# Kernel optimization log

Measured on AMD Instinct MI355X. Metric: run time of the kernel, lower is better.

Reference implementation:

```python
import jax, jax.numpy as jnp
import numpy as np

B, C, L, N, S = 32, 256, 512, 1024, 8  # batch, channels, seq_len, n_rois, output bins


def setup_inputs() -> dict:
    key = jax.random.key(0)
    k1, k2, k3 = jax.random.split(key, 3)
    sentences = jax.random.normal(k1, (B, C, L, 1), dtype=jnp.float32)
    rois = jnp.sort(jax.random.randint(k2, (N, 2), 0, L, dtype=jnp.int64), axis=1)
    # guarantee non-empty crop: x2 >= x1 + 1 (clamped into [0, L])
    x1 = jnp.minimum(rois[:, 0], L - 1)
    x2 = jnp.clip(rois[:, 1], x1 + 1, L)
    rois = jnp.stack([x1, x2], axis=1)
    roi_idx = jax.random.randint(k3, (N,), 0, B, dtype=jnp.int64)
    return {"sentences": sentences, "rois": rois, "roi_idx": roi_idx}


def reference(sentences, rois, roi_idx):
    # Gather per-ROI sentences; width dim is always sliced [0:1] -> drop it.
    x = sentences[roi_idx, :, :, 0]              # [N, C, L]
    x1 = rois[:, 0]                               # [N]
    x2 = rois[:, 1]                               # [N]
    lr = x2 - x1                                  # per-ROI crop length, >= 1
    pos = jnp.arange(L)[None, :]                  # [1, L]
    bins = []
    for j in range(S):  # fixed small loop over output bins
        # AdaptiveMaxPool bin j: [floor(j*lr/S), ceil((j+1)*lr/S)) offset by x1
        start = x1 + (j * lr) // S                # [N]
        end = x1 + ((j + 1) * lr + S - 1) // S    # [N]
        mask = (pos >= start[:, None]) & (pos < end[:, None])  # [N, L]
        masked = jnp.where(mask[:, None, :], x, -jnp.inf)       # [N, C, L]
        bins.append(masked.max(axis=-1))                         # [N, C]
    out = jnp.stack(bins, axis=-1)[..., None]     # [N, C, S, 1]
    return out
```

## Files before the change

kernel.cpp:

```cpp
#include <hip/hip_runtime.h>
#include <cfloat>

constexpr int Bc = 32;
constexpr int Cc = 256;
constexpr int Lc = 512;
constexpr int Nc = 1024;
constexpr int Sc = 8;

constexpr int CT     = 16;
constexpr int STRIDE = 516;

typedef float f4 __attribute__((ext_vector_type(4)));
typedef float f2 __attribute__((ext_vector_type(2)));

__global__ __launch_bounds__(256) void roi_pool_fused2(
    const float* __restrict__ sentences,
    const int*   __restrict__ rois,
    const int*   __restrict__ roi_idx,
    float*       __restrict__ out)
{
    __shared__ float rowbuf[CT * STRIDE];
    __shared__ int   list[Nc];
    __shared__ int   wcnt[16];

    const int bid  = blockIdx.x;
    const int b    = bid >> 5;
    const int ct   = (bid >> 1) & 15;
    const int half = bid & 1;
    const int c0   = ct * CT;

    const int tid  = threadIdx.x;
    const int lane = tid & 63;
    const int w    = tid >> 6;

    int myidx[4], mypos[4];
    #pragma unroll
    for (int q = 0; q < 4; ++q) {
        const int i = q * 256 + tid;
        const int v = roi_idx[i];
        const unsigned long long mask = __ballot(v == b);
        mypos[q] = __popcll(mask & ((1ull << lane) - 1ull));
        myidx[q] = (v == b) ? i : -1;
        if (lane == 0) wcnt[q * 4 + w] = __popcll(mask);
    }

    {
        const f4* src = (const f4*)(sentences + ((size_t)b * Cc + c0) * Lc);
        #pragma unroll
        for (int i = 0; i < (CT * Lc / 4) / 256; ++i) {
            const int idx = tid + i * 256;
            const int r   = idx >> 7;
            const int q   = idx & 127;
            f4 v = src[r * (Lc / 4) + q];
            *(f4*)(rowbuf + r * STRIDE + 4 * q) = v;
        }
    }
    __syncthreads();

    int wb0 = 0, wb1 = 0, wb2 = 0, wb3 = 0, run = 0;
    #pragma unroll
    for (int t = 0; t < 16; ++t) {
        if (t == w)      wb0 = run;
        if (t == 4 + w)  wb1 = run;
        if (t == 8 + w)  wb2 = run;
        if (t == 12 + w) wb3 = run;
        run += wcnt[t];
    }
    const int m = run;

    if (myidx[0] >= 0) list[wb0 + mypos[0]] = myidx[0];
    if (myidx[1] >= 0) list[wb1 + mypos[1]] = myidx[1];
    if (myidx[2] >= 0) list[wb2 + mypos[2]] = myidx[2];
    if (myidx[3] >= 0) list[wb3 + mypos[3]] = myidx[3];
    __syncthreads();

    const int rp = tid >> 7;
    const int cl = (tid >> 3) & 15;
    const int j  = tid & 7;
    const float* row = rowbuf + cl * STRIDE;

    for (int i = half + 2 * rp; i < m; i += 4) {
        const int n  = list[i];
        const int x1 = rois[2 * n];
        const int x2 = rois[2 * n + 1];
        const int lr = x2 - x1;
        const int s  = x1 + ((j * lr) >> 3);
        const int e  = x1 + (((j + 1) * lr + Sc - 1) >> 3);

        float m0 = -FLT_MAX, m1 = -FLT_MAX;
        int p = s;
        if (p & 1) { m0 = row[p]; ++p; }
        for (; p + 4 <= e; p += 4) {
            f2 a = *(const f2*)(row + p);
            f2 c = *(const f2*)(row + p + 2);
            m0 = fmaxf(m0, fmaxf(a.x, a.y));
            m1 = fmaxf(m1, fmaxf(c.x, c.y));
        }
        if (p + 2 <= e) {
            f2 a = *(const f2*)(row + p);
            m0 = fmaxf(m0, fmaxf(a.x, a.y));
            p += 2;
        }
        if (p < e) m0 = fmaxf(m0, row[p]);

        out[(size_t)n * (Cc * Sc) + (c0 + cl) * Sc + j] = fmaxf(m0, m1);
    }
}

extern "C" void kernel_launch(void* const* d_in, const int* in_sizes, int n_in,
                              void* d_out, int out_size, void* d_ws, size_t ws_size,
                              hipStream_t stream) {
    const float* sentences = (const float*)d_in[0];
    const int*   rois      = (const int*)d_in[1];
    const int*   roi_idx   = (const int*)d_in[2];
    float*       out       = (float*)d_out;

    roi_pool_fused2<<<Bc * (Cc / CT) * 2, 256, 0, stream>>>(sentences, rois, roi_idx, out);
}
```

Measured before the change: 19.71 us.

## Add 4-wide max pyramid level in shared memory and drop half-split blocks

While staging each channel tile into shared memory, the kernel now also stores a per-4-element max level. Each bin reduction then handles only the partial 4-element chunks at its ends with masked vector reads and takes the interior from the reduced level, which cuts LDS reads and max operations for long bins. The grid is halved: each block now processes all of its batch's ROIs instead of splitting them across two blocks, so the global staging of the tile is no longer duplicated. In exchange, fewer blocks are in flight, each block does more serial ROI iterations, and shared-memory use per block rises slightly.

```diff
diff --git a/kernel.cpp b/kernel.cpp
--- a/kernel.cpp
+++ b/kernel.cpp
@@ -11,24 +11,29 @@
 constexpr int STRIDE = 516;
 
 typedef float f4 __attribute__((ext_vector_type(4)));
-typedef float f2 __attribute__((ext_vector_type(2)));
 
-__global__ __launch_bounds__(256) void roi_pool_fused2(
+__device__ __forceinline__ float chunkmax(f4 v, int lo, int hi, float m) {
+    float a0 = (lo <= 0 && 0 < hi) ? v.x : -FLT_MAX;
+    float a1 = (lo <= 1 && 1 < hi) ? v.y : -FLT_MAX;
+    float a2 = (lo <= 2 && 2 < hi) ? v.z : -FLT_MAX;
+    float a3 = (lo <= 3 && 3 < hi) ? v.w : -FLT_MAX;
+    return fmaxf(fmaxf(m, fmaxf(a0, a1)), fmaxf(a2, a3));
+}
+
+__global__ __launch_bounds__(256) void roi_pool_pyr2(
     const float* __restrict__ sentences,
     const int*   __restrict__ rois,
     const int*   __restrict__ roi_idx,
     float*       __restrict__ out)
 {
     __shared__ float rowbuf[CT * STRIDE];
+    __shared__ float lvl1[CT * 128];
     __shared__ int   list[Nc];
     __shared__ int   wcnt[16];
 
     const int bid  = blockIdx.x;
-    const int b    = bid >> 5;
-    const int ct   = (bid >> 1) & 15;
-    const int half = bid & 1;
-    const int c0   = ct * CT;
-
+    const int b    = bid >> 4;
+    const int c0   = (bid & 15) * CT;
     const int tid  = threadIdx.x;
     const int lane = tid & 63;
     const int w    = tid >> 6;
@@ -53,6 +58,7 @@
             const int q   = idx & 127;
             f4 v = src[r * (Lc / 4) + q];
             *(f4*)(rowbuf + r * STRIDE + 4 * q) = v;
+            lvl1[r * 128 + q] = fmaxf(fmaxf(v.x, v.y), fmaxf(v.z, v.w));
         }
     }
     __syncthreads();
@@ -78,8 +84,9 @@
     const int cl = (tid >> 3) & 15;
     const int j  = tid & 7;
     const float* row = rowbuf + cl * STRIDE;
+    const float* lv  = lvl1 + cl * 128;
 
-    for (int i = half + 2 * rp; i < m; i += 4) {
+    for (int i = rp; i < m; i += 2) {
         const int n  = list[i];
         const int x1 = rois[2 * n];
         const int x2 = rois[2 * n + 1];
@@ -87,23 +94,21 @@
         const int s  = x1 + ((j * lr) >> 3);
         const int e  = x1 + (((j + 1) * lr + Sc - 1) >> 3);
 
-        float m0 = -FLT_MAX, m1 = -FLT_MAX;
-        int p = s;
-        if (p & 1) { m0 = row[p]; ++p; }
-        for (; p + 4 <= e; p += 4) {
-            f2 a = *(const f2*)(row + p);
-            f2 c = *(const f2*)(row + p + 2);
-            m0 = fmaxf(m0, fmaxf(a.x, a.y));
-            m1 = fmaxf(m1, fmaxf(c.x, c.y));
+        const int qs = s >> 2;
+        const int qe = e >> 2;
+
+        f4 hv = *(const f4*)(row + 4 * qs);
+        float mm = chunkmax(hv, s & 3, min(4, e - 4 * qs), -FLT_MAX);
+
+        for (int q = qs + 1; q < qe; ++q)
+            mm = fmaxf(mm, lv[q]);
+
+        if ((e & 3) && qe > qs) {
+            f4 tv = *(const f4*)(row + 4 * qe);
+            mm = chunkmax(tv, 0, e & 3, mm);
         }
-        if (p + 2 <= e) {
-            f2 a = *(const f2*)(row + p);
-            m0 = fmaxf(m0, fmaxf(a.x, a.y));
-            p += 2;
-        }
-        if (p < e) m0 = fmaxf(m0, row[p]);
 
-        out[(size_t)n * (Cc * Sc) + (c0 + cl) * Sc + j] = fmaxf(m0, m1);
+        out[(size_t)n * (Cc * Sc) + (c0 + cl) * Sc + j] = mm;
     }
 }
 
@@ -115,5 +120,5 @@
     const int*   roi_idx   = (const int*)d_in[2];
     float*       out       = (float*)d_out;
 
-    roi_pool_fused2<<<Bc * (Cc / CT) * 2, 256, 0, stream>>>(sentences, rois, roi_idx, out);
+    roi_pool_pyr2<<<Bc * (Cc / CT), 256, 0, stream>>>(sentences, rois, roi_idx, out);
 }
```

Measured after the change: 24.17 us. +22.6%, slower.
